# Performance work log

Hardware: AMD Instinct MI355X
Metric: run time of the kernel (lower is better)

Reference implementation:

```python
import jax, jax.numpy as jnp
import numpy as np

HEADS = 8

def setup_inputs() -> dict:
    key = jax.random.key(0)
    ks = jax.random.split(key, 6)
    b, c, w, h = 4, 512, 48, 48
    qc, vc = 512, 512
    s = 1.0 / np.sqrt(c)  # orthogonal-init-like scale for 1x1 conv weights
    return {
        "x": jax.random.normal(ks[0], (b, c, w, h), dtype=jnp.float32),
        "Wq": jax.random.normal(ks[1], (qc, c), dtype=jnp.float32) * s,
        "Wk": jax.random.normal(ks[2], (qc, c), dtype=jnp.float32) * s,
        "Wv": jax.random.normal(ks[3], (vc, c), dtype=jnp.float32) * s,
        "Wsc": jax.random.normal(ks[4], (vc, c), dtype=jnp.float32) * s,
        "gamma": jax.random.normal(ks[5], (1, vc, 1, 1), dtype=jnp.float32),
    }


def reference(x, Wq, Wk, Wv, Wsc, gamma):
    b, c, w, h = x.shape
    n = w * h
    dq = Wq.shape[0] // HEADS
    dv = Wv.shape[0] // HEADS
    # 1x1 convs are channel matmuls
    q = jnp.einsum('bchw,oc->bohw', x, Wq).reshape(b, HEADS, dq, n)
    k = jnp.einsum('bchw,oc->bohw', x, Wk).reshape(b, HEADS, dq, n)
    v = jnp.einsum('bchw,oc->bohw', x, Wv).reshape(b, HEADS, dv, n)
    # attention scores over spatial tokens (no scaling in original)
    attn = jax.nn.softmax(jnp.einsum('bhdn,bhdm->bhnm', q, k), axis=-1)
    out = jnp.einsum('bhnm,bhdm->bnhd', attn, v)  # (b, n, heads, dv)
    out = out.reshape(b, w, h, HEADS * dv).transpose(0, 3, 1, 2)  # head-major channels
    sc = jnp.einsum('bchw,oc->bohw', x, Wsc)
    return gamma * out + sc
```

## Files before the change

kernel.cpp:

```cpp
#include <hip/hip_runtime.h>

#define HEADS 8
static constexpr int BSZ = 4;
static constexpr int CCH = 512;
static constexpr int NSP = 2304;
static constexpr int DH  = 64;

typedef _Float16 f16x8 __attribute__((ext_vector_type(8)));
typedef float f32x4 __attribute__((ext_vector_type(4)));
typedef float f32x16 __attribute__((ext_vector_type(16)));
typedef int i32x4 __attribute__((ext_vector_type(4)));
typedef unsigned short u16;
typedef unsigned int u32;

__device__ __forceinline__ u16 f2h(float f) {
  _Float16 h = (_Float16)f;
  return __builtin_bit_cast(u16, h);
}

__device__ __forceinline__ float fexp2(float x) {
  return __builtin_amdgcn_exp2f(x);
}

__device__ __forceinline__ void gl_lds16(const void* g, void* l) {
  __builtin_amdgcn_global_load_lds(
      (const __attribute__((address_space(1))) u32*)g,
      (__attribute__((address_space(3))) u32*)l, 16, 0, 0);
}

__global__ void k_cvt_w(const float* __restrict__ w0, const float* __restrict__ w1,
                        const float* __restrict__ w2, const float* __restrict__ w3,
                        u16* __restrict__ dst) {
  int wsel = blockIdx.y;
  const float* src = wsel == 0 ? w0 : wsel == 1 ? w1 : wsel == 2 ? w2 : w3;
  int i = (blockIdx.x * 256 + threadIdx.x) * 4;
  float4 v = *(const float4*)(src + i);
  ushort4 o;
  o.x = f2h(v.x); o.y = f2h(v.y); o.z = f2h(v.z); o.w = f2h(v.w);
  *(ushort4*)(dst + (size_t)wsel * CCH * CCH + i) = o;
}

__global__ void k_cvt_x(const float* __restrict__ x, u16* __restrict__ xT) {
  __shared__ u16 t[64][66];
  int b = blockIdx.z, c0 = blockIdx.y * 64, n0 = blockIdx.x * 64;
  int col = threadIdx.x & 63, rb = threadIdx.x >> 6;
#pragma unroll
  for (int rr = 0; rr < 16; rr++) {
    int r = rr * 4 + rb;
    t[r][col] = f2h(x[((size_t)b * CCH + c0 + r) * NSP + n0 + col]);
  }
  __syncthreads();
#pragma unroll
  for (int rr = 0; rr < 16; rr++) {
    int r = rr * 4 + rb;
    xT[((size_t)b * NSP + n0 + r) * CCH + c0 + col] = t[col][r];
  }
}

__global__ __launch_bounds__(256) void k_proj(const u16* __restrict__ Wall,
    const u16* __restrict__ xT, u16* __restrict__ Qo, u16* __restrict__ Ko,
    u16* __restrict__ Vo, float* __restrict__ SCo) {
  __shared__ u16 smem[17408];
  u16* At = smem;
  u16* Bt = smem + 8192;
  int z = blockIdx.z, b = z >> 2, wsel = z & 3;
  int o0 = blockIdx.y * 128, n0 = blockIdx.x * 128;
  int tid = threadIdx.x, lane = tid & 63, wv = tid >> 6;
  int wr = wv >> 1, wc = wv & 1;
  const u16* Asrc = Wall + (size_t)wsel * CCH * CCH + (size_t)o0 * CCH;
  const u16* Bsrc = xT + ((size_t)b * NSP + n0) * CCH;
  f32x4 acc[4][4] = {};
  for (int kc = 0; kc < CCH; kc += 64) {
    __syncthreads();
#pragma unroll
    for (int i = 0; i < 4; i++) {
      int ch = (wv * 4 + i) * 64 + lane;
      int row = ch >> 3, cc = ch & 7;
      gl_lds16(Asrc + (size_t)row * CCH + kc + ((cc ^ (row & 7)) << 3), At + (wv * 4 + i) * 512);
      gl_lds16(Bsrc + (size_t)row * CCH + kc + ((cc ^ (row & 7)) << 3), Bt + (wv * 4 + i) * 512);
    }
    __syncthreads();
#pragma unroll
    for (int ks = 0; ks < 2; ks++) {
      f16x8 af[4], bfr[4];
#pragma unroll
      for (int f = 0; f < 4; f++) {
        int orow = wr * 64 + f * 16 + (lane & 15);
        int nrow = wc * 64 + f * 16 + (lane & 15);
        int k8 = (lane >> 4) + ks * 4;
        af[f]  = *(const f16x8*)(At + orow * 64 + ((k8 ^ (orow & 7)) << 3));
        bfr[f] = *(const f16x8*)(Bt + nrow * 64 + ((k8 ^ (nrow & 7)) << 3));
      }
#pragma unroll
      for (int i = 0; i < 4; i++)
#pragma unroll
        for (int j = 0; j < 4; j++)
          acc[i][j] = __builtin_amdgcn_mfma_f32_16x16x32_f16(af[i], bfr[j], acc[i][j], 0, 0, 0);
    }
  }
  if (wsel >= 2) {
#pragma unroll
    for (int i = 0; i < 4; i++)
#pragma unroll
      for (int j = 0; j < 4; j++)
#pragma unroll
        for (int r = 0; r < 4; r++) {
          int o = o0 + wr * 64 + i * 16 + ((lane >> 4) << 2) + r;
          int n = n0 + wc * 64 + j * 16 + (lane & 15);
          size_t idx = ((size_t)b * CCH + o) * NSP + n;
          if (wsel == 3) SCo[idx] = acc[i][j][r];
          else           Vo[idx]  = f2h(acc[i][j][r]);
        }
  } else {
    __syncthreads();
    u16* stash = smem;
    float qs = (wsel == 0) ? 1.4426950408889634f : 1.0f;
#pragma unroll
    for (int i = 0; i < 4; i++)
#pragma unroll
      for (int j = 0; j < 4; j++)
#pragma unroll
        for (int r = 0; r < 4; r++) {
          int ol = wr * 64 + i * 16 + ((lane >> 4) << 2) + r;
          int nl = wc * 64 + j * 16 + (lane & 15);
          stash[nl * 136 + ol] = f2h(acc[i][j][r] * qs);
        }
    __syncthreads();
    u16* dst = wsel ? Ko : Qo;
    int hl = tid >> 7, nn = tid & 127;
    int h = (o0 >> 6) + hl;
    size_t base = ((size_t)(b * HEADS + h) * NSP + n0 + nn) * DH;
#pragma unroll
    for (int c2 = 0; c2 < 8; c2++)
      *(int4*)(dst + base + c2 * 8) = *(const int4*)(stash + nn * 136 + hl * 64 + c2 * 8);
  }
}

__device__ __forceinline__ void stage_kv256(const u16* Ksrc, const u16* Vsrc,
                                            u16* Kb, u16* Vb, int m0, int gid) {
#pragma unroll
  for (int i = 0; i < 2; i++) {
    int ch = i * 256 + gid;
    int row = ch >> 3, p = ch & 7;
    int cc = p ^ (row & 7) ^ (((row >> 3) & 3) << 1);
    gl_lds16(Ksrc + (size_t)(m0 + row) * DH + (cc << 3), Kb + ch * 8);
    gl_lds16(Vsrc + (size_t)row * NSP + m0 + (cc << 3), Vb + ch * 8);
  }
}

__global__ __launch_bounds__(512, 2) void k_attn(const u16* __restrict__ Qw,
    const u16* __restrict__ Kw, const u16* __restrict__ Vw,
    const float* __restrict__ gamma, float* __restrict__ out) {
  __shared__ u16 smem[32768];
  int qt = blockIdx.x, bh = blockIdx.y;
  int b = bh >> 3, h = bh & 7;
  int tid = threadIdx.x, lane = tid & 63, wv = tid >> 6;
  int l31 = lane & 31, hi = lane >> 5;
  int qh = wv & 3, tp = wv >> 2;
  int gid = tid & 255;
  int q0w = qt * 128 + qh * 32;
  const u16* Ksrc = Kw + (size_t)bh * NSP * DH;
  const u16* Vsrc = Vw + ((size_t)b * CCH + h * DH) * NSP;
  u16* Kb = smem + tp * 16384;
  u16* Vb = Kb + 8192;
  int kswz = (l31 & 7) ^ (((l31 >> 3) & 3) << 1);

  f16x8 qf[4];
  const u16* Qbase = Qw + ((size_t)bh * NSP + q0w + l31) * DH + hi * 8;
#pragma unroll
  for (int kd = 0; kd < 4; kd++)
    qf[kd] = *(const f16x8*)(Qbase + kd * 16);

  float mrun = -1e30f, lrun = 0.f;
  f32x16 acc0 = {}, acc1 = {};

  stage_kv256(Ksrc, Vsrc, Kb, Vb, tp * 64, gid);
  __syncthreads();

  const int NT = NSP / 128;
  for (int it = 0; it < NT; it++) {
    int cur = it & 1;
    if (it + 1 < NT)
      stage_kv256(Ksrc, Vsrc, Kb + (cur ^ 1) * 4096, Vb + (cur ^ 1) * 4096,
                  (tp + 2 * (it + 1)) * 64, gid);
    const u16* Kc = Kb + cur * 4096;
    const u16* Vc = Vb + cur * 4096;

    f32x16 s0 = {}, s1 = {};
#pragma unroll
    for (int kd = 0; kd < 4; kd++) {
      int pk = ((2 * kd + hi) ^ kswz) << 3;
      f16x8 k0 = *(const f16x8*)(Kc + l31 * 64 + pk);
      f16x8 k1 = *(const f16x8*)(Kc + (32 + l31) * 64 + pk);
      s0 = __builtin_amdgcn_mfma_f32_32x32x16_f16(k0, qf[kd], s0, 0, 0, 0);
      s1 = __builtin_amdgcn_mfma_f32_32x32x16_f16(k1, qf[kd], s1, 0, 0, 0);
    }

    float a8[8];
#pragma unroll
    for (int i = 0; i < 8; i++)
      a8[i] = fmaxf(fmaxf(s0[2 * i], s0[2 * i + 1]), fmaxf(s1[2 * i], s1[2 * i + 1]));
    float tm = fmaxf(fmaxf(fmaxf(a8[0], a8[1]), fmaxf(a8[2], a8[3])),
                     fmaxf(fmaxf(a8[4], a8[5]), fmaxf(a8[6], a8[7])));
    tm = fmaxf(tm, __shfl_xor(tm, 32));
    if (__any(tm > mrun + 11.5f)) {
      float mnew = fmaxf(mrun, tm);
      float scl = fexp2(mrun - mnew);
      mrun = mnew;
      lrun *= scl;
#pragma unroll
      for (int r = 0; r < 16; r++) {
        float sq = __shfl(scl, (r & 3) + 8 * (r >> 2) + 4 * hi);
        acc0[r] *= sq;
        acc1[r] *= sq;
      }
    }
    float tsp[4] = {0.f, 0.f, 0.f, 0.f};
    u32 P2[2][4][2];
#pragma unroll
    for (int s2 = 0; s2 < 4; s2++)
#pragma unroll
      for (int c = 0; c < 2; c++) {
        float a0 = fexp2(s0[4 * s2 + 2 * c] - mrun);
        float b0 = fexp2(s0[4 * s2 + 2 * c + 1] - mrun);
        float a1 = fexp2(s1[4 * s2 + 2 * c] - mrun);
        float b1 = fexp2(s1[4 * s2 + 2 * c + 1] - mrun);
        tsp[s2] += (a0 + b0) + (a1 + b1);
        P2[0][s2][c] = __builtin_bit_cast(u32, __builtin_amdgcn_cvt_pkrtz(a0, b0));
        P2[1][s2][c] = __builtin_bit_cast(u32, __builtin_amdgcn_cvt_pkrtz(a1, b1));
      }
    float ts = (tsp[0] + tsp[1]) + (tsp[2] + tsp[3]);
    ts += __shfl_xor(ts, 32);
    lrun += ts;

#pragma unroll
    for (int s = 0; s < 4; s++) {
      int blk = s >> 1, par = s & 1;
      int T[4];
#pragma unroll
      for (int c = 0; c < 2; c++) {
        int x = (int)P2[blk][2 * par][c];
        int y = (int)P2[blk][2 * par + 1][c];
        int xs = __shfl_xor(x, 32);
        int ys = __shfl_xor(y, 32);
        T[c]     = hi ? ys : x;
        T[c + 2] = hi ? y  : xs;
      }
      f16x8 pa = __builtin_bit_cast(f16x8, (i32x4){T[0], T[1], T[2], T[3]});
      int pv = ((2 * s + hi) ^ kswz) << 3;
      {
        f16x8 vb = *(const f16x8*)(Vc + l31 * 64 + pv);
        acc0 = __builtin_amdgcn_mfma_f32_32x32x16_f16(pa, vb, acc0, 0, 0, 0);
      }
      {
        f16x8 vb = *(const f16x8*)(Vc + (32 + l31) * 64 + pv);
        acc1 = __builtin_amdgcn_mfma_f32_32x32x16_f16(pa, vb, acc1, 0, 0, 0);
      }
    }
    __syncthreads();
  }

  float* sf = (float*)smem;
  if (tp) {
#pragma unroll
    for (int r = 0; r < 16; r++) {
      sf[qh * 2048 + r * 64 + lane] = acc0[r];
      sf[qh * 2048 + (16 + r) * 64 + lane] = acc1[r];
    }
    if (lane < 32) {
      sf[8192 + qh * 64 + l31] = mrun;
      sf[8192 + qh * 64 + 32 + l31] = lrun;
    }
  }
  __syncthreads();
  if (!tp) {
    float mb = sf[8192 + qh * 64 + l31];
    float lb = sf[8192 + qh * 64 + 32 + l31];
    float M = fmaxf(mrun, mb);
    float fa = fexp2(mrun - M), fb = fexp2(mb - M);
    float linv = 1.0f / (lrun * fa + lb * fb);
    fa *= linv; fb *= linv;
    float faq[16], fbq[16];
#pragma unroll
    for (int r = 0; r < 16; r++) {
      int qloc = (r & 3) + 8 * (r >> 2) + 4 * hi;
      faq[r] = __shfl(fa, qloc);
      fbq[r] = __shfl(fb, qloc);
    }
    size_t outbase = ((size_t)b * CCH + h * DH) * NSP;
#pragma unroll
    for (int dblk = 0; dblk < 2; dblk++) {
      int d = dblk * 32 + l31;
      float g = gamma[h * DH + d];
      float* orow = out + outbase + (size_t)d * NSP + q0w;
#pragma unroll
      for (int s2 = 0; s2 < 4; s2++) {
        int n = 8 * s2 + 4 * hi;
        f32x4 o;
#pragma unroll
        for (int t = 0; t < 4; t++) {
          int r = 4 * s2 + t;
          float oa = dblk ? acc1[r] : acc0[r];
          float ob = sf[qh * 2048 + (dblk * 16 + r) * 64 + lane];
          o[t] = (oa * faq[r] + ob * fbq[r]) * g;
        }
        f32x4 sc = *(const f32x4*)(orow + n);
        *(f32x4*)(orow + n) = o + sc;
      }
    }
  }
}

extern "C" void kernel_launch(void* const* d_in, const int* in_sizes, int n_in,
                              void* d_out, int out_size, void* d_ws, size_t ws_size,
                              hipStream_t stream) {
  const float* x     = (const float*)d_in[0];
  const float* Wq    = (const float*)d_in[1];
  const float* Wk    = (const float*)d_in[2];
  const float* Wv    = (const float*)d_in[3];
  const float* Wsc   = (const float*)d_in[4];
  const float* gamma = (const float*)d_in[5];
  float* out = (float*)d_out;

  u16* xT   = (u16*)d_ws;
  u16* Wall = xT + (size_t)BSZ * NSP * CCH;
  u16* Qw   = Wall + (size_t)4 * CCH * CCH;
  u16* Kw   = Qw + (size_t)BSZ * CCH * NSP;
  u16* Vw   = Kw + (size_t)BSZ * CCH * NSP;

  hipLaunchKernelGGL(k_cvt_w, dim3(CCH * CCH / 1024, 4), dim3(256), 0, stream,
                     Wq, Wk, Wv, Wsc, Wall);
  hipLaunchKernelGGL(k_cvt_x, dim3(NSP / 64, CCH / 64, BSZ), dim3(256), 0, stream, x, xT);
  hipLaunchKernelGGL(k_proj, dim3(NSP / 128, CCH / 128, BSZ * 4), dim3(256), 0, stream,
                     Wall, xT, Qw, Kw, Vw, out);
  hipLaunchKernelGGL(k_attn, dim3(NSP / 128, BSZ * HEADS), dim3(512), 0, stream,
                     Qw, Kw, Vw, gamma, out);
}
```

Measured before the change: 157.0 us.

## Shrink attention blocks to 256 threads with 32-key tiles and higher occupancy

The attention kernel moves from 512-thread blocks covering 128 queries to 256-thread blocks covering 64 queries. Each warp now processes 32-key tiles instead of 64, which halves the score registers per warp. LDS use is halved, the LDS swizzles for K and V are rewritten, and launch bounds allow 5 blocks per CU, with s_setprio raised around the MFMA sections. This aims to improve occupancy and latency hiding, at the cost of twice as many loop iterations and barriers, and twice as many K/V tile loads from global memory.

```diff
diff --git a/kernel.cpp b/kernel.cpp
--- a/kernel.cpp
+++ b/kernel.cpp
@@ -136,34 +136,34 @@
   }
 }
 
-__device__ __forceinline__ void stage_kv256(const u16* Ksrc, const u16* Vsrc,
-                                            u16* Kb, u16* Vb, int m0, int gid) {
+__device__ __forceinline__ void stage_kv(const u16* Ksrc, const u16* Vsrc,
+                                         u16* Kb, u16* Vb, int m0, int gid) {
 #pragma unroll
   for (int i = 0; i < 2; i++) {
-    int ch = i * 256 + gid;
-    int row = ch >> 3, p = ch & 7;
-    int cc = p ^ (row & 7) ^ (((row >> 3) & 3) << 1);
-    gl_lds16(Ksrc + (size_t)(m0 + row) * DH + (cc << 3), Kb + ch * 8);
-    gl_lds16(Vsrc + (size_t)row * NSP + m0 + (cc << 3), Vb + ch * 8);
-  }
-}
-
-__global__ __launch_bounds__(512, 2) void k_attn(const u16* __restrict__ Qw,
+    int ch = i * 128 + gid;
+    int mk = ch >> 3, pk = ch & 7;
+    gl_lds16(Ksrc + (size_t)(m0 + mk) * DH + ((pk ^ (mk & 7)) << 3), Kb + ch * 8);
+    int dv = ch >> 2, pv = ch & 3;
+    gl_lds16(Vsrc + (size_t)dv * NSP + m0 + ((pv ^ ((dv >> 1) & 3)) << 3), Vb + ch * 8);
+  }
+}
+
+__global__ __launch_bounds__(256, 5) void k_attn(const u16* __restrict__ Qw,
     const u16* __restrict__ Kw, const u16* __restrict__ Vw,
     const float* __restrict__ gamma, float* __restrict__ out) {
-  __shared__ u16 smem[32768];
+  __shared__ u16 smem[16384];
   int qt = blockIdx.x, bh = blockIdx.y;
   int b = bh >> 3, h = bh & 7;
   int tid = threadIdx.x, lane = tid & 63, wv = tid >> 6;
   int l31 = lane & 31, hi = lane >> 5;
-  int qh = wv & 3, tp = wv >> 2;
-  int gid = tid & 255;
-  int q0w = qt * 128 + qh * 32;
+  int qh = wv & 1, tp = wv >> 1;
+  int gid = tid & 127;
+  int q0w = qt * 64 + qh * 32;
   const u16* Ksrc = Kw + (size_t)bh * NSP * DH;
   const u16* Vsrc = Vw + ((size_t)b * CCH + h * DH) * NSP;
-  u16* Kb = smem + tp * 16384;
-  u16* Vb = Kb + 8192;
-  int kswz = (l31 & 7) ^ (((l31 >> 3) & 3) << 1);
+  u16* Kb = smem + tp * 8192;
+  int kswz = l31 & 7;
+  int vswz = (l31 >> 1) & 3;
 
   f16x8 qf[4];
   const u16* Qbase = Qw + ((size_t)bh * NSP + q0w + l31) * DH + hi * 8;
@@ -174,32 +174,30 @@
   float mrun = -1e30f, lrun = 0.f;
   f32x16 acc0 = {}, acc1 = {};
 
-  stage_kv256(Ksrc, Vsrc, Kb, Vb, tp * 64, gid);
+  stage_kv(Ksrc, Vsrc, Kb, Kb + 2048, tp * 32, gid);
   __syncthreads();
 
-  const int NT = NSP / 128;
+  const int NT = NSP / 64;
   for (int it = 0; it < NT; it++) {
     int cur = it & 1;
     if (it + 1 < NT)
-      stage_kv256(Ksrc, Vsrc, Kb + (cur ^ 1) * 4096, Vb + (cur ^ 1) * 4096,
-                  (tp + 2 * (it + 1)) * 64, gid);
+      stage_kv(Ksrc, Vsrc, Kb + (cur ^ 1) * 4096, Kb + (cur ^ 1) * 4096 + 2048,
+               (tp + 2 * (it + 1)) * 32, gid);
     const u16* Kc = Kb + cur * 4096;
-    const u16* Vc = Vb + cur * 4096;
-
-    f32x16 s0 = {}, s1 = {};
+    const u16* Vc = Kc + 2048;
+
+    f32x16 s0 = {};
+    __builtin_amdgcn_s_setprio(1);
 #pragma unroll
     for (int kd = 0; kd < 4; kd++) {
-      int pk = ((2 * kd + hi) ^ kswz) << 3;
-      f16x8 k0 = *(const f16x8*)(Kc + l31 * 64 + pk);
-      f16x8 k1 = *(const f16x8*)(Kc + (32 + l31) * 64 + pk);
+      f16x8 k0 = *(const f16x8*)(Kc + l31 * 64 + (((2 * kd + hi) ^ kswz) << 3));
       s0 = __builtin_amdgcn_mfma_f32_32x32x16_f16(k0, qf[kd], s0, 0, 0, 0);
-      s1 = __builtin_amdgcn_mfma_f32_32x32x16_f16(k1, qf[kd], s1, 0, 0, 0);
-    }
+    }
+    __builtin_amdgcn_s_setprio(0);
 
     float a8[8];
 #pragma unroll
-    for (int i = 0; i < 8; i++)
-      a8[i] = fmaxf(fmaxf(s0[2 * i], s0[2 * i + 1]), fmaxf(s1[2 * i], s1[2 * i + 1]));
+    for (int i = 0; i < 8; i++) a8[i] = fmaxf(s0[2 * i], s0[2 * i + 1]);
     float tm = fmaxf(fmaxf(fmaxf(a8[0], a8[1]), fmaxf(a8[2], a8[3])),
                      fmaxf(fmaxf(a8[4], a8[5]), fmaxf(a8[6], a8[7])));
     tm = fmaxf(tm, __shfl_xor(tm, 32));
@@ -215,47 +213,44 @@
         acc1[r] *= sq;
       }
     }
-    float tsp[4] = {0.f, 0.f, 0.f, 0.f};
-    u32 P2[2][4][2];
+    float ts = 0.f;
+    u32 P2[4][2];
 #pragma unroll
     for (int s2 = 0; s2 < 4; s2++)
 #pragma unroll
       for (int c = 0; c < 2; c++) {
-        float a0 = fexp2(s0[4 * s2 + 2 * c] - mrun);
-        float b0 = fexp2(s0[4 * s2 + 2 * c + 1] - mrun);
-        float a1 = fexp2(s1[4 * s2 + 2 * c] - mrun);
-        float b1 = fexp2(s1[4 * s2 + 2 * c + 1] - mrun);
-        tsp[s2] += (a0 + b0) + (a1 + b1);
-        P2[0][s2][c] = __builtin_bit_cast(u32, __builtin_amdgcn_cvt_pkrtz(a0, b0));
-        P2[1][s2][c] = __builtin_bit_cast(u32, __builtin_amdgcn_cvt_pkrtz(a1, b1));
-      }
-    float ts = (tsp[0] + tsp[1]) + (tsp[2] + tsp[3]);
+        float a = fexp2(s0[4 * s2 + 2 * c] - mrun);
+        float bb = fexp2(s0[4 * s2 + 2 * c + 1] - mrun);
+        ts += a + bb;
+        P2[s2][c] = __builtin_bit_cast(u32, __builtin_amdgcn_cvt_pkrtz(a, bb));
+      }
     ts += __shfl_xor(ts, 32);
     lrun += ts;
 
 #pragma unroll
-    for (int s = 0; s < 4; s++) {
-      int blk = s >> 1, par = s & 1;
+    for (int s = 0; s < 2; s++) {
       int T[4];
 #pragma unroll
       for (int c = 0; c < 2; c++) {
-        int x = (int)P2[blk][2 * par][c];
-        int y = (int)P2[blk][2 * par + 1][c];
+        int x = (int)P2[2 * s][c];
+        int y = (int)P2[2 * s + 1][c];
         int xs = __shfl_xor(x, 32);
         int ys = __shfl_xor(y, 32);
         T[c]     = hi ? ys : x;
         T[c + 2] = hi ? y  : xs;
       }
       f16x8 pa = __builtin_bit_cast(f16x8, (i32x4){T[0], T[1], T[2], T[3]});
-      int pv = ((2 * s + hi) ^ kswz) << 3;
+      int pv = ((2 * s + hi) ^ vswz) << 3;
+      __builtin_amdgcn_s_setprio(1);
       {
-        f16x8 vb = *(const f16x8*)(Vc + l31 * 64 + pv);
+        f16x8 vb = *(const f16x8*)(Vc + l31 * 32 + pv);
         acc0 = __builtin_amdgcn_mfma_f32_32x32x16_f16(pa, vb, acc0, 0, 0, 0);
       }
       {
-        f16x8 vb = *(const f16x8*)(Vc + (32 + l31) * 64 + pv);
+        f16x8 vb = *(const f16x8*)(Vc + (32 + l31) * 32 + pv);
         acc1 = __builtin_amdgcn_mfma_f32_32x32x16_f16(pa, vb, acc1, 0, 0, 0);
       }
+      __builtin_amdgcn_s_setprio(0);
     }
     __syncthreads();
   }
@@ -268,14 +263,14 @@
       sf[qh * 2048 + (16 + r) * 64 + lane] = acc1[r];
     }
     if (lane < 32) {
-      sf[8192 + qh * 64 + l31] = mrun;
-      sf[8192 + qh * 64 + 32 + l31] = lrun;
+      sf[4096 + qh * 64 + l31] = mrun;
+      sf[4096 + qh * 64 + 32 + l31] = lrun;
     }
   }
   __syncthreads();
   if (!tp) {
-    float mb = sf[8192 + qh * 64 + l31];
-    float lb = sf[8192 + qh * 64 + 32 + l31];
+    float mb = sf[4096 + qh * 64 + l31];
+    float lb = sf[4096 + qh * 64 + 32 + l31];
     float M = fmaxf(mrun, mb);
     float fa = fexp2(mrun - M), fb = fexp2(mb - M);
     float linv = 1.0f / (lrun * fa + lb * fb);
@@ -333,6 +328,6 @@
   hipLaunchKernelGGL(k_cvt_x, dim3(NSP / 64, CCH / 64, BSZ), dim3(256), 0, stream, x, xT);
   hipLaunchKernelGGL(k_proj, dim3(NSP / 128, CCH / 128, BSZ * 4), dim3(256), 0, stream,
                      Wall, xT, Qw, Kw, Vw, out);
-  hipLaunchKernelGGL(k_attn, dim3(NSP / 128, BSZ * HEADS), dim3(512), 0, stream,
+  hipLaunchKernelGGL(k_attn, dim3(NSP / 64, BSZ * HEADS), dim3(256), 0, stream,
                      Qw, Kw, Vw, gamma, out);
 }
```

After: 195.2 us. 24.3% more time.
